# Kernel optimization log

Measured on AMD Instinct MI355X. Metric: run time of the kernel, lower is better.

Reference implementation:

```python
import jax, jax.numpy as jnp
import numpy as np

INIT_IN = 32      # init_input_dim (raw feature dim of x)
D = 128           # output_dim == init_output_dim
IN_DIM = 2 * D + INIT_IN  # input_dim = 288
NUM_LAYERS = 4    # loop runs num_layers-1 = 3 rounds
NV = 50000        # num variables
NC = 50000        # num constraints
DEG = 16          # padded neighbor list length


def _linear_params(key, out_dim, in_dim):
    k1, k2 = jax.random.split(key)
    bound = 1.0 / np.sqrt(in_dim)
    W = jax.random.uniform(k1, (out_dim, in_dim), minval=-bound, maxval=bound, dtype=jnp.float32)
    b = jax.random.uniform(k2, (out_dim,), minval=-bound, maxval=bound, dtype=jnp.float32)
    return W, b


def setup_inputs() -> dict:
    key = jax.random.key(0)
    ks = jax.random.split(key, 8)
    x = jax.random.normal(ks[0], (NV + NC, INIT_IN), dtype=jnp.float32)
    var_constr_index = jax.random.randint(ks[1], (NV, DEG), 0, NC).astype(jnp.int64)
    constr_var_index = jax.random.randint(ks[2], (NC, DEG), 0, NV).astype(jnp.int64)
    W_iv, b_iv = _linear_params(ks[3], D, INIT_IN)
    W_ic, b_ic = _linear_params(ks[4], D, INIT_IN)
    W_v, b_v = _linear_params(ks[5], D, IN_DIM)
    W_c, b_c = _linear_params(ks[6], D, IN_DIM)
    W_q, b_q = _linear_params(ks[7], 1, 2 * D)
    return dict(x=x, var_constr_index=var_constr_index, constr_var_index=constr_var_index,
                W_iv=W_iv, b_iv=b_iv, W_ic=W_ic, b_ic=b_ic,
                W_v=W_v, b_v=b_v, W_c=W_c, b_c=b_c, W_q=W_q, b_q=b_q)


def reference(x, var_constr_index, constr_var_index,
              W_iv, b_iv, W_ic, b_ic, W_v, b_v, W_c, b_c, W_q, b_q):
    nv = var_constr_index.shape[0]
    var_feat = x[:nv]          # [NV, INIT_IN]
    con_feat = x[nv:]          # [NC, INIT_IN]
    # layer zero init
    lv = var_feat @ W_iv.T + b_iv   # [NV, D]
    lc = con_feat @ W_ic.T + b_ic   # [NC, D]
    zeros = jnp.zeros((1, D), dtype=lv.dtype)
    for _ in range(1, NUM_LAYERS):
        lv_pad = jnp.concatenate([lv, zeros], axis=0)  # -1 pad idx -> zeros row
        lc_pad = jnp.concatenate([lc, zeros], axis=0)
        # constraint update: gather variable neighbors, sum, fuse with linear
        c_agg = lv_pad[constr_var_index].sum(axis=1)   # [NC, D]
        lc_new = jnp.concatenate([c_agg, lc, con_feat], axis=1) @ W_c.T + b_c
        # variable update uses OLD (pre-update) constraint features (lc_pad)
        v_agg = lc_pad[var_constr_index].sum(axis=1)   # [NV, D]
        lv = jnp.concatenate([v_agg, lv, var_feat], axis=1) @ W_v.T + b_v
        lc = lc_new
    # embedding_Q: global sum of variable features broadcast to each variable
    g = lv.sum(axis=0, keepdims=True)                  # [1, D]
    g = jnp.broadcast_to(g, lv.shape)                  # [NV, D]
    Q = jnp.concatenate([g, lv], axis=1) @ W_q.T + b_q # [NV, 1]
    return Q
```

## Files before the change

kernel.cpp:

```cpp
#include <hip/hip_runtime.h>

#define NVV 50000
#define NCC 50000
#define DD 128
#define FIN 32
#define INDIM 288
#define DEG 16

typedef unsigned short u16;
typedef unsigned char u8;
typedef unsigned int u32;
typedef __attribute__((ext_vector_type(8))) short short8;
typedef __attribute__((ext_vector_type(4))) float f32x4;
typedef __attribute__((ext_vector_type(2))) float f32x2;

constexpr int NT = 256;
constexpr int GRID_HALF = 782;

__device__ __forceinline__ float b2f(u16 b) {
  union { u32 u; float f; } v; v.u = ((u32)b) << 16; return v.f;
}
__device__ __forceinline__ u16 f2b(float f) {
  union { float f; u32 u; } v; v.f = f;
  u32 u = v.u + 0x7FFFu + ((v.u >> 16) & 1u);
  return (u16)(u >> 16);
}
__device__ __forceinline__ float bits2f(u32 u) {
  union { u32 u; float f; } v; v.u = u; return v.f;
}
__device__ __forceinline__ u32 pack2(float a, float b) {
  return (u32)f2b(a) | ((u32)f2b(b) << 16);
}
__device__ __forceinline__ u8 f2fp8(float f) {
  return (u8)(__builtin_amdgcn_cvt_pk_fp8_f32(f, f, 0, false) & 0xFF);
}

__device__ __forceinline__ void dma16(const void* g, void* l) {
  __builtin_amdgcn_global_load_lds(
      (__attribute__((address_space(1))) void*)g,
      (__attribute__((address_space(3))) void*)l, 16, 0, 0);
}

__device__ __forceinline__ short8 fp8x8_to_bf16frag(u32 lo, u32 hi) {
  f32x2 a0 = __builtin_amdgcn_cvt_pk_f32_fp8(lo, false);
  f32x2 a1 = __builtin_amdgcn_cvt_pk_f32_fp8(lo, true);
  f32x2 a2 = __builtin_amdgcn_cvt_pk_f32_fp8(hi, false);
  f32x2 a3 = __builtin_amdgcn_cvt_pk_f32_fp8(hi, true);
  u32 ab[4] = { pack2(a0.x, a0.y), pack2(a1.x, a1.y),
                pack2(a2.x, a2.y), pack2(a3.x, a3.y) };
  return *(short8*)ab;
}

__global__ __launch_bounds__(NT) void swizzle_all(
    const float* __restrict__ Wv, const float* __restrict__ Wc,
    const float* __restrict__ Wiv, const float* __restrict__ Wic,
    u16* __restrict__ Wvsw, u16* __restrict__ Wcsw,
    u16* __restrict__ Wivsw, u16* __restrict__ Wicsw, float* __restrict__ g)
{
  int t = blockIdx.x * NT + threadIdx.x;
  if (t >= 10240) {
    int gi = t - 10240;
    if (gi < 128) g[gi] = 0.f;
    return;
  }
  const float* W; u16* out; int f; int indim;
  if (t < 4608)       { W = Wv;  out = Wvsw;  f = t;        indim = INDIM; }
  else if (t < 9216)  { W = Wc;  out = Wcsw;  f = t - 4608; indim = INDIM; }
  else if (t < 9728)  { W = Wiv; out = Wivsw; f = t - 9216; indim = FIN; }
  else                { W = Wic; out = Wicsw; f = t - 9728; indim = FIN; }
  int lane = f & 63, nt = (f >> 6) & 7, kt = f >> 9;
  int li = lane & 15, quad = lane >> 4;
  const float* src = W + (size_t)(nt * 16 + li) * indim + kt * 32 + quad * 8;
  float4 a = *(const float4*)src, b = *(const float4*)(src + 4);
  u32 o[4] = { pack2(a.x, a.y), pack2(a.z, a.w), pack2(b.x, b.y), pack2(b.z, b.w) };
  *(int4*)(out + (size_t)f * 8) = *(int4*)o;
}

__global__ __launch_bounds__(NT) void init_fused(
    const float* __restrict__ x,
    const u16* __restrict__ Wivsw, const u16* __restrict__ Wicsw,
    const float* __restrict__ b_iv, const float* __restrict__ b_ic,
    u8* __restrict__ lv08, u8* __restrict__ lc08,
    u16* __restrict__ xvb, u16* __restrict__ xcb)
{
  __shared__ char smem8[4 * 2048];
  const int bid = blockIdx.x;
  const bool isC = bid >= GRID_HALF;
  const int lb = isC ? bid - GRID_HALF : bid;
  const float* xs = x + (isC ? (size_t)NVV * FIN : 0);
  const u16* Wsw = isC ? Wicsw : Wivsw;
  const float* bias = isC ? b_ic : b_iv;
  u8*  out8 = isC ? lc08 : lv08;
  u16* feat = isC ? xcb : xvb;
  const int nrows = isC ? NCC : NVV;

  const int t = threadIdx.x;
  const int r0 = lb * 64;

  {
    const int row = r0 + (t >> 2);
    if (row < nrows) {
      const float* src = xs + (size_t)row * FIN + (t & 3) * 8;
      float4 a = *(const float4*)src, b = *(const float4*)(src + 4);
      u32 o[4] = { pack2(a.x, a.y), pack2(a.z, a.w), pack2(b.x, b.y), pack2(b.z, b.w) };
      *(int4*)(feat + (size_t)row * FIN + (t & 3) * 8) = *(int4*)o;
    }
  }

  const int wave = t >> 6, l = t & 63;
  const int quad = l >> 4, li = l & 15;
  const int r0w = r0 + wave * 16;
  int rowm = r0w + li;
  if (rowm >= nrows) rowm = nrows - 1;

  short8 afrag;
  {
    const float* src = xs + (size_t)rowm * FIN + quad * 8;
    float4 a = *(const float4*)src, b = *(const float4*)(src + 4);
    u32 o[4] = { pack2(a.x, a.y), pack2(a.z, a.w), pack2(b.x, b.y), pack2(b.z, b.w) };
    afrag = *(short8*)o;
  }

  f32x4 acc[8];
#pragma unroll
  for (int nt = 0; nt < 8; ++nt) acc[nt] = (f32x4){0.f, 0.f, 0.f, 0.f};
#pragma unroll
  for (int nt = 0; nt < 8; ++nt) {
    short8 b = *(const short8*)(Wsw + (size_t)(nt * 64 + l) * 8);
    acc[nt] = __builtin_amdgcn_mfma_f32_16x16x32_bf16(afrag, b, acc[nt], 0, 0, 0);
  }

  u8* s8 = (u8*)(smem8 + wave * 2048);
#pragma unroll
  for (int nt = 0; nt < 8; ++nt) {
    const int col = nt * 16 + li;
    const float bv = bias[col];
#pragma unroll
    for (int i = 0; i < 4; ++i)
      s8[(quad * 4 + i) * 128 + col] = f2fp8(acc[nt][i] + bv);
  }
  asm volatile("s_waitcnt lgkmcnt(0)" ::: "memory");
  if (r0w < nrows) {
    const char* s8c = (const char*)s8 + l * 32;
    char* g8 = (char*)out8 + (size_t)r0w * 128 + l * 32;
#pragma unroll
    for (int c = 0; c < 2; ++c) *(int4*)(g8 + c * 16) = *(const int4*)(s8c + c * 16);
  }
}

__device__ __forceinline__ void issue_group8(const char* gp, int offj, char* slotbase) {
  const char* rp = gp + (size_t)(u32)offj;
  dma16(rp, slotbase);
  dma16(rp + 64, slotbase + 1024);
}
__device__ __forceinline__ void consume_slot8(const char* slot, int li, int quad,
                                              float (&sagg)[4][8]) {
  const int c2 = quad >> 1, half = quad & 1;
#pragma unroll
  for (int kt = 0; kt < 4; ++kt) {
    int4 v = *(const int4*)(slot + (2 * kt + c2) * 256 + li * 16);
    u32 w0 = half ? (u32)v.z : (u32)v.x;
    u32 w1 = half ? (u32)v.w : (u32)v.y;
    f32x2 a0 = __builtin_amdgcn_cvt_pk_f32_fp8(w0, false);
    f32x2 a1 = __builtin_amdgcn_cvt_pk_f32_fp8(w0, true);
    f32x2 a2 = __builtin_amdgcn_cvt_pk_f32_fp8(w1, false);
    f32x2 a3 = __builtin_amdgcn_cvt_pk_f32_fp8(w1, true);
    sagg[kt][0] += a0.x; sagg[kt][1] += a0.y;
    sagg[kt][2] += a1.x; sagg[kt][3] += a1.y;
    sagg[kt][4] += a2.x; sagg[kt][5] += a2.y;
    sagg[kt][6] += a3.x; sagg[kt][7] += a3.y;
  }
}

template <bool GACC>
__device__ __forceinline__ void layer_body(
    const u8* __restrict__ gsrc, const u8* __restrict__ self8,
    const u16* __restrict__ feat, const int* __restrict__ idx,
    const u16* __restrict__ Wsw, const float* __restrict__ bias,
    u16* __restrict__ out16, u8* __restrict__ out8, float* __restrict__ g,
    int nrows, int bid, int t, char* smem)
{
  const int wave = t >> 6, l = t & 63;
  const int quad = l >> 4, li = l & 15;
  const int r0w = bid * 64 + wave * 16;

  int4 iv;
  {
    int rload = r0w + (l >> 2);
    if (rload >= nrows) rload = nrows - 1;
    iv = *(const int4*)(idx + (size_t)rload * DEG + (l & 3) * 4);
  }
  int off[DEG];
#pragma unroll
  for (int j = 0; j < DEG; ++j) {
    int comp = ((j & 3) == 0) ? iv.x : ((j & 3) == 1) ? iv.y : ((j & 3) == 2) ? iv.z : iv.w;
    off[j] = __shfl(comp, (li << 2) + (j >> 2)) << 7;
  }

  int rowm = r0w + li;
  if (rowm >= nrows) rowm = nrows - 1;

  f32x4 acc[8];
#pragma unroll
  for (int nt = 0; nt < 8; ++nt) acc[nt] = (f32x4){0.f, 0.f, 0.f, 0.f};

  {
    short8 a = *(const short8*)(feat + (size_t)rowm * FIN + quad * 8);
#pragma unroll
    for (int nt = 0; nt < 8; ++nt) {
      short8 b = *(const short8*)(Wsw + (size_t)((8 * 8 + nt) * 64 + l) * 8);
      acc[nt] = __builtin_amdgcn_mfma_f32_16x16x32_bf16(a, b, acc[nt], 0, 0, 0);
    }
  }
#pragma unroll
  for (int k2 = 0; k2 < 4; ++k2) {
    const u32* sp = (const u32*)(self8 + (size_t)rowm * DD + k2 * 32 + quad * 8);
    short8 a = fp8x8_to_bf16frag(sp[0], sp[1]);
#pragma unroll
    for (int nt = 0; nt < 8; ++nt) {
      short8 b = *(const short8*)(Wsw + (size_t)(((4 + k2) * 8 + nt) * 64 + l) * 8);
      acc[nt] = __builtin_amdgcn_mfma_f32_16x16x32_bf16(a, b, acc[nt], 0, 0, 0);
    }
  }

  float sagg[4][8];
#pragma unroll
  for (int k2 = 0; k2 < 4; ++k2)
#pragma unroll
    for (int p = 0; p < 8; ++p) sagg[k2][p] = 0.f;

  asm volatile("s_waitcnt vmcnt(0)" ::: "memory");

  char* wb = smem + wave * 8192;
  const char* gp = (const char*)gsrc + quad * 16;
  issue_group8(gp, off[0], wb);
  issue_group8(gp, off[1], wb + 2048);
  issue_group8(gp, off[2], wb + 4096);
  issue_group8(gp, off[3], wb + 6144);
#define R8_STEP(J, IJ)                                               \
  asm volatile("s_waitcnt vmcnt(6)" ::: "memory");                   \
  consume_slot8(wb + ((J) & 3) * 2048, li, quad, sagg);              \
  asm volatile("s_waitcnt lgkmcnt(0)" ::: "memory");                 \
  issue_group8(gp, off[IJ], wb + ((J) & 3) * 2048);
#define R8_TAIL(J, VN)                                               \
  asm volatile("s_waitcnt vmcnt(" #VN ")" ::: "memory");             \
  consume_slot8(wb + ((J) & 3) * 2048, li, quad, sagg);
  R8_STEP(0, 4)  R8_STEP(1, 5)  R8_STEP(2, 6)  R8_STEP(3, 7)
  R8_STEP(4, 8)  R8_STEP(5, 9)  R8_STEP(6, 10) R8_STEP(7, 11)
  R8_STEP(8, 12) R8_STEP(9, 13) R8_STEP(10, 14) R8_STEP(11, 15)
  R8_TAIL(12, 6) R8_TAIL(13, 4) R8_TAIL(14, 2)  R8_TAIL(15, 0)
#undef R8_STEP
#undef R8_TAIL

#pragma unroll
  for (int k2 = 0; k2 < 4; ++k2) {
    u32 a_bits[4];
#pragma unroll
    for (int p = 0; p < 4; ++p) a_bits[p] = pack2(sagg[k2][2 * p], sagg[k2][2 * p + 1]);
    short8 a = *(short8*)a_bits;
#pragma unroll
    for (int nt = 0; nt < 8; ++nt) {
      short8 b = *(const short8*)(Wsw + (size_t)((k2 * 8 + nt) * 64 + l) * 8);
      acc[nt] = __builtin_amdgcn_mfma_f32_16x16x32_bf16(a, b, acc[nt], 0, 0, 0);
    }
  }

  asm volatile("s_waitcnt lgkmcnt(0)" ::: "memory");
  if constexpr (!GACC) {
    u8* s8 = (u8*)wb;
#pragma unroll
    for (int nt = 0; nt < 8; ++nt) {
      const int col = nt * 16 + li;
      const float bv = bias[col];
#pragma unroll
      for (int i = 0; i < 4; ++i)
        s8[(quad * 4 + i) * 128 + col] = f2fp8(acc[nt][i] + bv);
    }
    asm volatile("s_waitcnt lgkmcnt(0)" ::: "memory");
    if (r0w < nrows) {
      const char* s8c = (const char*)s8 + l * 32;
      char* g8 = (char*)out8 + (size_t)r0w * 128 + l * 32;
#pragma unroll
      for (int c = 0; c < 2; ++c) *(int4*)(g8 + c * 16) = *(const int4*)(s8c + c * 16);
    }
  } else {
    const int rbase = r0w + quad * 4;
    float colsum[8];
#pragma unroll
    for (int nt = 0; nt < 8; ++nt) {
      const int col = nt * 16 + li;
      const float bv = bias[col];
      colsum[nt] = 0.f;
#pragma unroll
      for (int i = 0; i < 4; ++i) {
        const int row = rbase + i;
        float v = acc[nt][i] + bv;
        if (row < nrows) {
          out16[(size_t)row * DD + col] = f2b(v);
          colsum[nt] += v;
        }
      }
    }
#pragma unroll
    for (int nt = 0; nt < 8; ++nt) {
      colsum[nt] += __shfl_xor(colsum[nt], 16);
      colsum[nt] += __shfl_xor(colsum[nt], 32);
    }
    __syncthreads();
    float* gsum = (float*)smem;
    if (quad == 0) {
#pragma unroll
      for (int nt = 0; nt < 8; ++nt) gsum[wave * 128 + nt * 16 + li] = colsum[nt];
    }
    __syncthreads();
    if (t < 128) {
      float tot = gsum[t] + gsum[128 + t] + gsum[256 + t] + gsum[384 + t];
      atomicAdd(&g[t], tot);
    }
  }
}

template <bool GACC>
__global__ __launch_bounds__(NT, 2) void layer_merged(
    const u8* gsrcC, const u8* selfC, const u16* featC, const int* idxC,
    const u16* WswC, const float* biasC, u16* out16C, u8* out8C, int nrowsC,
    const u8* gsrcV, const u8* selfV, const u16* featV, const int* idxV,
    const u16* WswV, const float* biasV, u16* out16V, u8* out8V, int nrowsV,
    float* g, int c_blocks)
{
  __shared__ char smem[32768];
  const int bid = blockIdx.x;
  const int t = threadIdx.x;
  if (bid < c_blocks)
    layer_body<GACC>(gsrcC, selfC, featC, idxC, WswC, biasC, out16C, out8C,
                     g, nrowsC, bid, t, smem);
  else
    layer_body<GACC>(gsrcV, selfV, featV, idxV, WswV, biasV, out16V, out8V,
                     g, nrowsV, bid - c_blocks, t, smem);
}

__global__ __launch_bounds__(NT) void final_kernel(
    const u16* __restrict__ lv, const float* __restrict__ g,
    const float* __restrict__ Wq, const float* __restrict__ bq,
    float* __restrict__ out)
{
  const int t = threadIdx.x, wave = t >> 6, l = t & 63;
  const float2 wg = *(const float2*)(Wq + 2 * l);
  const float2 wl = *(const float2*)(Wq + DD + 2 * l);
  const float2 gv = *(const float2*)(g + 2 * l);
  float q = wg.x * gv.x + wg.y * gv.y;
#pragma unroll
  for (int off = 32; off; off >>= 1) q += __shfl_down(q, off);
  const float qg = __shfl(q, 0) + bq[0];

  const int r0w = blockIdx.x * 64 + wave * 16;
#pragma unroll
  for (int i = 0; i < 16; ++i) {
    const int r = r0w + i;
    if (r >= NVV) break;
    u32 v = *(const u32*)(lv + (size_t)r * DD + 2 * l);
    float p = wl.x * b2f((u16)(v & 0xFFFF)) + wl.y * b2f((u16)(v >> 16));
#pragma unroll
    for (int off = 32; off; off >>= 1) p += __shfl_down(p, off);
    if (l == 0) out[r] = qg + p;
  }
}

extern "C" void kernel_launch(void* const* d_in, const int* in_sizes, int n_in,
                              void* d_out, int out_size, void* d_ws, size_t ws_size,
                              hipStream_t stream) {
  const float* x    = (const float*)d_in[0];
  const int*   vci  = (const int*)d_in[1];
  const int*   cvi  = (const int*)d_in[2];
  const float* W_iv = (const float*)d_in[3];
  const float* b_iv = (const float*)d_in[4];
  const float* W_ic = (const float*)d_in[5];
  const float* b_ic = (const float*)d_in[6];
  const float* W_v  = (const float*)d_in[7];
  const float* b_v  = (const float*)d_in[8];
  const float* W_c  = (const float*)d_in[9];
  const float* b_c  = (const float*)d_in[10];
  const float* W_q  = (const float*)d_in[11];
  const float* b_q  = (const float*)d_in[12];
  float* out = (float*)d_out;

  float* g = (float*)d_ws;
  u16* base = (u16*)((char*)d_ws + 512);
  const size_t nodef = (size_t)NVV * DD;
  u16* xb    = base;
  u16* Wvsw  = xb + (size_t)(NVV + NCC) * FIN;
  u16* Wcsw  = Wvsw + (size_t)DD * INDIM;
  u16* Wivsw = Wcsw + (size_t)DD * INDIM;
  u16* Wicsw = Wivsw + (size_t)DD * FIN;
  u16* lv1   = Wicsw + (size_t)DD * FIN;
  u8*  lv08  = (u8*)(lv1 + nodef);
  u8*  lc08  = lv08 + nodef;
  u8*  lv18  = lc08 + nodef;
  u8*  lc18  = lv18 + nodef;
  u8*  lv28  = lc18 + nodef;
  u8*  lc28  = lv28 + nodef;
  u16* xvb   = xb;
  u16* xcb   = xb + (size_t)NVV * FIN;

  dim3 blk(NT);

  swizzle_all<<<41, blk, 0, stream>>>(W_v, W_c, W_iv, W_ic, Wvsw, Wcsw, Wivsw, Wicsw, g);
  init_fused<<<2 * GRID_HALF, blk, 0, stream>>>(x, Wivsw, Wicsw, b_iv, b_ic,
                                                lv08, lc08, xvb, xcb);

  layer_merged<false><<<2 * GRID_HALF, blk, 0, stream>>>(
      lv08, lc08, xcb, cvi, Wcsw, b_c, nullptr, lc18, NCC,
      lc08, lv08, xvb, vci, Wvsw, b_v, nullptr, lv18, NVV, g, GRID_HALF);
  layer_merged<false><<<2 * GRID_HALF, blk, 0, stream>>>(
      lv18, lc18, xcb, cvi, Wcsw, b_c, nullptr, lc28, NCC,
      lc18, lv18, xvb, vci, Wvsw, b_v, nullptr, lv28, NVV, g, GRID_HALF);
  layer_merged<true><<<GRID_HALF, blk, 0, stream>>>(
      lc28, lv28, xvb, vci, Wvsw, b_v, lv1, nullptr, NVV,
      lc28, lv28, xvb, vci, Wvsw, b_v, lv1, nullptr, NVV, g, 0);

  final_kernel<<<GRID_HALF, blk, 0, stream>>>(lv1, g, W_q, b_q, out);
}
```

Baseline: 280.5 us.

## Store raw input features as fp8 and issue neighbor gathers before self GEMM

The cached raw node features are now written in fp8 instead of bf16, which halves the bytes read for that operand in every layer. In each layer the neighbor gather DMAs are issued before the self-feature and raw-feature MFMA work, so the gather latency overlaps with matrix compute. The cost is extra precision loss on the raw input features, plus an fp8-to-bf16 conversion when they are loaded.

```diff
diff --git a/kernel.cpp b/kernel.cpp
--- a/kernel.cpp
+++ b/kernel.cpp
@@ -24,9 +24,6 @@
   union { float f; u32 u; } v; v.f = f;
   u32 u = v.u + 0x7FFFu + ((v.u >> 16) & 1u);
   return (u16)(u >> 16);
-}
-__device__ __forceinline__ float bits2f(u32 u) {
-  union { u32 u; float f; } v; v.u = u; return v.f;
 }
 __device__ __forceinline__ u32 pack2(float a, float b) {
   return (u32)f2b(a) | ((u32)f2b(b) << 16);
@@ -49,6 +46,14 @@
   u32 ab[4] = { pack2(a0.x, a0.y), pack2(a1.x, a1.y),
                 pack2(a2.x, a2.y), pack2(a3.x, a3.y) };
   return *(short8*)ab;
+}
+__device__ __forceinline__ void f32x8_to_fp8x8(float4 a, float4 b, u32* o) {
+  u32 lo = 0, hi = 0;
+  lo = __builtin_amdgcn_cvt_pk_fp8_f32(a.x, a.y, lo, false);
+  lo = __builtin_amdgcn_cvt_pk_fp8_f32(a.z, a.w, lo, true);
+  hi = __builtin_amdgcn_cvt_pk_fp8_f32(b.x, b.y, hi, false);
+  hi = __builtin_amdgcn_cvt_pk_fp8_f32(b.z, b.w, hi, true);
+  o[0] = lo; o[1] = hi;
 }
 
 __global__ __launch_bounds__(NT) void swizzle_all(
@@ -81,7 +86,7 @@
     const u16* __restrict__ Wivsw, const u16* __restrict__ Wicsw,
     const float* __restrict__ b_iv, const float* __restrict__ b_ic,
     u8* __restrict__ lv08, u8* __restrict__ lc08,
-    u16* __restrict__ xvb, u16* __restrict__ xcb)
+    u8* __restrict__ xvb8, u8* __restrict__ xcb8)
 {
   __shared__ char smem8[4 * 2048];
   const int bid = blockIdx.x;
@@ -91,7 +96,7 @@
   const u16* Wsw = isC ? Wicsw : Wivsw;
   const float* bias = isC ? b_ic : b_iv;
   u8*  out8 = isC ? lc08 : lv08;
-  u16* feat = isC ? xcb : xvb;
+  u8*  feat8 = isC ? xcb8 : xvb8;
   const int nrows = isC ? NCC : NVV;
 
   const int t = threadIdx.x;
@@ -101,9 +106,9 @@
     const int row = r0 + (t >> 2);
     if (row < nrows) {
       const float* src = xs + (size_t)row * FIN + (t & 3) * 8;
-      float4 a = *(const float4*)src, b = *(const float4*)(src + 4);
-      u32 o[4] = { pack2(a.x, a.y), pack2(a.z, a.w), pack2(b.x, b.y), pack2(b.z, b.w) };
-      *(int4*)(feat + (size_t)row * FIN + (t & 3) * 8) = *(int4*)o;
+      u32 o[2];
+      f32x8_to_fp8x8(*(const float4*)src, *(const float4*)(src + 4), o);
+      *(int2*)(feat8 + (size_t)row * FIN + (t & 3) * 8) = *(int2*)o;
     }
   }
 
@@ -175,7 +180,7 @@
 template <bool GACC>
 __device__ __forceinline__ void layer_body(
     const u8* __restrict__ gsrc, const u8* __restrict__ self8,
-    const u16* __restrict__ feat, const int* __restrict__ idx,
+    const u8* __restrict__ feat8, const int* __restrict__ idx,
     const u16* __restrict__ Wsw, const float* __restrict__ bias,
     u16* __restrict__ out16, u8* __restrict__ out8, float* __restrict__ g,
     int nrows, int bid, int t, char* smem)
@@ -200,43 +205,44 @@
   int rowm = r0w + li;
   if (rowm >= nrows) rowm = nrows - 1;
 
-  f32x4 acc[8];
-#pragma unroll
-  for (int nt = 0; nt < 8; ++nt) acc[nt] = (f32x4){0.f, 0.f, 0.f, 0.f};
-
-  {
-    short8 a = *(const short8*)(feat + (size_t)rowm * FIN + quad * 8);
-#pragma unroll
-    for (int nt = 0; nt < 8; ++nt) {
-      short8 b = *(const short8*)(Wsw + (size_t)((8 * 8 + nt) * 64 + l) * 8);
-      acc[nt] = __builtin_amdgcn_mfma_f32_16x16x32_bf16(a, b, acc[nt], 0, 0, 0);
-    }
-  }
-#pragma unroll
-  for (int k2 = 0; k2 < 4; ++k2) {
-    const u32* sp = (const u32*)(self8 + (size_t)rowm * DD + k2 * 32 + quad * 8);
-    short8 a = fp8x8_to_bf16frag(sp[0], sp[1]);
-#pragma unroll
-    for (int nt = 0; nt < 8; ++nt) {
-      short8 b = *(const short8*)(Wsw + (size_t)(((4 + k2) * 8 + nt) * 64 + l) * 8);
-      acc[nt] = __builtin_amdgcn_mfma_f32_16x16x32_bf16(a, b, acc[nt], 0, 0, 0);
-    }
-  }
-
-  float sagg[4][8];
-#pragma unroll
-  for (int k2 = 0; k2 < 4; ++k2)
-#pragma unroll
-    for (int p = 0; p < 8; ++p) sagg[k2][p] = 0.f;
-
-  asm volatile("s_waitcnt vmcnt(0)" ::: "memory");
-
   char* wb = smem + wave * 8192;
   const char* gp = (const char*)gsrc + quad * 16;
+  asm volatile("s_waitcnt vmcnt(0)" ::: "memory");
   issue_group8(gp, off[0], wb);
   issue_group8(gp, off[1], wb + 2048);
   issue_group8(gp, off[2], wb + 4096);
   issue_group8(gp, off[3], wb + 6144);
+
+  f32x4 acc[8];
+#pragma unroll
+  for (int nt = 0; nt < 8; ++nt) acc[nt] = (f32x4){0.f, 0.f, 0.f, 0.f};
+
+  {
+    const u32* fp = (const u32*)(feat8 + (size_t)rowm * FIN + quad * 8);
+    short8 a = fp8x8_to_bf16frag(fp[0], fp[1]);
+#pragma unroll
+    for (int nt = 0; nt < 8; ++nt) {
+      short8 b = *(const short8*)(Wsw + (size_t)((8 * 8 + nt) * 64 + l) * 8);
+      acc[nt] = __builtin_amdgcn_mfma_f32_16x16x32_bf16(a, b, acc[nt], 0, 0, 0);
+    }
+  }
+#pragma unroll
+  for (int k2 = 0; k2 < 4; ++k2) {
+    const u32* sp = (const u32*)(self8 + (size_t)rowm * DD + k2 * 32 + quad * 8);
+    short8 a = fp8x8_to_bf16frag(sp[0], sp[1]);
+#pragma unroll
+    for (int nt = 0; nt < 8; ++nt) {
+      short8 b = *(const short8*)(Wsw + (size_t)(((4 + k2) * 8 + nt) * 64 + l) * 8);
+      acc[nt] = __builtin_amdgcn_mfma_f32_16x16x32_bf16(a, b, acc[nt], 0, 0, 0);
+    }
+  }
+
+  float sagg[4][8];
+#pragma unroll
+  for (int k2 = 0; k2 < 4; ++k2)
+#pragma unroll
+    for (int p = 0; p < 8; ++p) sagg[k2][p] = 0.f;
+
 #define R8_STEP(J, IJ)                                               \
   asm volatile("s_waitcnt vmcnt(6)" ::: "memory");                   \
   consume_slot8(wb + ((J) & 3) * 2048, li, quad, sagg);              \
@@ -322,9 +328,9 @@
 
 template <bool GACC>
 __global__ __launch_bounds__(NT, 2) void layer_merged(
-    const u8* gsrcC, const u8* selfC, const u16* featC, const int* idxC,
+    const u8* gsrcC, const u8* selfC, const u8* featC, const int* idxC,
     const u16* WswC, const float* biasC, u16* out16C, u8* out8C, int nrowsC,
-    const u8* gsrcV, const u8* selfV, const u16* featV, const int* idxV,
+    const u8* gsrcV, const u8* selfV, const u8* featV, const int* idxV,
     const u16* WswV, const float* biasV, u16* out16V, u8* out8V, int nrowsV,
     float* g, int c_blocks)
 {
@@ -385,38 +391,37 @@
   float* out = (float*)d_out;
 
   float* g = (float*)d_ws;
-  u16* base = (u16*)((char*)d_ws + 512);
+  u16* wbase = (u16*)((char*)d_ws + 512);
   const size_t nodef = (size_t)NVV * DD;
-  u16* xb    = base;
-  u16* Wvsw  = xb + (size_t)(NVV + NCC) * FIN;
+  u16* Wvsw  = wbase;
   u16* Wcsw  = Wvsw + (size_t)DD * INDIM;
   u16* Wivsw = Wcsw + (size_t)DD * INDIM;
   u16* Wicsw = Wivsw + (size_t)DD * FIN;
   u16* lv1   = Wicsw + (size_t)DD * FIN;
-  u8*  lv08  = (u8*)(lv1 + nodef);
+  u8*  xvb8  = (u8*)(lv1 + nodef);
+  u8*  xcb8  = xvb8 + (size_t)NVV * FIN;
+  u8*  lv08  = xcb8 + (size_t)NCC * FIN;
   u8*  lc08  = lv08 + nodef;
   u8*  lv18  = lc08 + nodef;
   u8*  lc18  = lv18 + nodef;
   u8*  lv28  = lc18 + nodef;
   u8*  lc28  = lv28 + nodef;
-  u16* xvb   = xb;
-  u16* xcb   = xb + (size_t)NVV * FIN;
 
   dim3 blk(NT);
 
   swizzle_all<<<41, blk, 0, stream>>>(W_v, W_c, W_iv, W_ic, Wvsw, Wcsw, Wivsw, Wicsw, g);
   init_fused<<<2 * GRID_HALF, blk, 0, stream>>>(x, Wivsw, Wicsw, b_iv, b_ic,
-                                                lv08, lc08, xvb, xcb);
+                                                lv08, lc08, xvb8, xcb8);
 
   layer_merged<false><<<2 * GRID_HALF, blk, 0, stream>>>(
-      lv08, lc08, xcb, cvi, Wcsw, b_c, nullptr, lc18, NCC,
-      lc08, lv08, xvb, vci, Wvsw, b_v, nullptr, lv18, NVV, g, GRID_HALF);
+      lv08, lc08, xcb8, cvi, Wcsw, b_c, nullptr, lc18, NCC,
+      lc08, lv08, xvb8, vci, Wvsw, b_v, nullptr, lv18, NVV, g, GRID_HALF);
   layer_merged<false><<<2 * GRID_HALF, blk, 0, stream>>>(
-      lv18, lc18, xcb, cvi, Wcsw, b_c, nullptr, lc28, NCC,
-      lc18, lv18, xvb, vci, Wvsw, b_v, nullptr, lv28, NVV, g, GRID_HALF);
+      lv18, lc18, xcb8, cvi, Wcsw, b_c, nullptr, lc28, NCC,
+      lc18, lv18, xvb8, vci, Wvsw, b_v, nullptr, lv28, NVV, g, GRID_HALF);
   layer_merged<true><<<GRID_HALF, blk, 0, stream>>>(
-      lc28, lv28, xvb, vci, Wvsw, b_v, lv1, nullptr, NVV,
-      lc28, lv28, xvb, vci, Wvsw, b_v, lv1, nullptr, NVV, g, 0);
+      lc28, lv28, xvb8, vci, Wvsw, b_v, lv1, nullptr, NVV,
+      lc28, lv28, xvb8, vci, Wvsw, b_v, lv1, nullptr, NVV, g, 0);
 
   final_kernel<<<GRID_HALF, blk, 0, stream>>>(lv1, g, W_q, b_q, out);
 }
```

After: 278.8 us. No clear change (-0.6%).
